# Kernel optimization log

Measured on AMD Instinct MI355X. Metric: run time of the kernel, lower is better.

## Reference

```python
import jax, jax.numpy as jnp
import numpy as np

# Fixed LeNet C3 connection table: input channel i feeds these 10 output channels.
CONN = [[0, 4, 5, 6, 9, 10, 11, 12, 14, 15],
        [0, 1, 5, 6, 7, 10, 11, 12, 13, 15],
        [0, 1, 2, 6, 7, 8, 11, 13, 14, 15],
        [1, 2, 3, 6, 7, 8, 9, 12, 14, 15],
        [2, 3, 4, 7, 8, 9, 10, 12, 13, 15],
        [3, 4, 5, 8, 9, 10, 11, 13, 14, 15]]
# Static scatter indices: (out_channel, in_channel) pairs, 60 total.
_ROWS = np.concatenate([np.asarray(l, np.int32) for l in CONN])  # out-channel ids
_COLS = np.repeat(np.arange(6, dtype=np.int32), 10)              # in-channel ids


def setup_inputs() -> dict:
    key = jax.random.key(0)
    k1, k2 = jax.random.split(key)
    x = jax.random.normal(k1, (64, 6, 256, 256), jnp.float32)
    # kaiming-uniform-ish scale for 6*5*5 fan-in
    weight = jax.random.normal(k2, (10, 6, 5, 5), jnp.float32) * 0.1
    bias = jnp.full((1, 16, 1, 1), 0.01, jnp.float32)
    return {"x": x, "weight": weight, "bias": bias}


def reference(x, weight, bias):
    # Fold the per-input-channel loop + scatter-add into one dense [16,6,5,5]
    # kernel with zeros where the connection table is absent. Each iteration i
    # of the original adds conv(x[:,i], weight[j,i]) to out channel CONN[i][j].
    w_flat = weight.transpose(1, 0, 2, 3).reshape(60, 5, 5)  # ordered (i, j)
    w_full = jnp.zeros((16, 6, 5, 5), weight.dtype).at[_ROWS, _COLS].set(w_flat)
    # Bias for channel c is added once per list containing c -> multiply by count.
    counts = jnp.zeros((16,), weight.dtype).at[_ROWS].add(1.0)
    out = jax.lax.conv_general_dilated(
        x, w_full, window_strides=(1, 1), padding='VALID',
        dimension_numbers=('NCHW', 'OIHW', 'NCHW'))
    return out + bias * counts.reshape(1, 16, 1, 1)
```

## Files before the change

kernel.cpp:

```cpp
#include <hip/hip_runtime.h>
#include <hip/hip_fp16.h>

typedef _Float16 f16x8 __attribute__((ext_vector_type(8)));
typedef float f32x4 __attribute__((ext_vector_type(4)));

__device__ constexpr int CONN[6][10] = {
    {0, 4, 5, 6, 9, 10, 11, 12, 14, 15},
    {0, 1, 5, 6, 7, 10, 11, 12, 13, 15},
    {0, 1, 2, 6, 7, 8, 11, 13, 14, 15},
    {1, 2, 3, 6, 7, 8, 9, 12, 14, 15},
    {2, 3, 4, 7, 8, 9, 10, 12, 13, 15},
    {3, 4, 5, 8, 9, 10, 11, 13, 14, 15}};

__device__ constexpr int CNT[16] = {3,3,3,3,3,3,4,4,4,4,4,4,4,4,4,6};

__device__ __forceinline__ f16x8 u4_to_h8(uint4 u) { f16x8 r; __builtin_memcpy(&r, &u, 16); return r; }

#define PITCH_DW 132
#define PLANE_DW (17 * 132)

__global__ void prep_A(const float* __restrict__ w, unsigned short* __restrict__ Wp) {
    int t = blockIdx.x * 256 + threadIdx.x;
    if (t >= 5120) return;
    int j = t & 7, lane = (t >> 3) & 63, ks = t >> 9;
    int ch = lane & 15, kb = lane >> 4;
    float val = 0.f;
    if (kb < 3 && j < 5) {
        int ii = 2 * kb + (ks >= 5 ? 1 : 0);
        int r  = (ks >= 5) ? ks - 5 : ks;
        for (int jj = 0; jj < 10; ++jj)
            if (CONN[ii][jj] == ch) val = w[jj * 150 + ii * 25 + r * 5 + j];
    }
    __half h = __float2half(val);
    unsigned short u; __builtin_memcpy(&u, &h, 2);
    Wp[t] = u;
}

__global__ __launch_bounds__(256, 3) void c3_mfma(
    const float* __restrict__ x, const unsigned short* __restrict__ Wp,
    const float* __restrict__ bias, float* __restrict__ out)
{
    __shared__ unsigned s_lds[6 * PLANE_DW];

    const int tid = threadIdx.x;
    const int id = (blockIdx.x & 7) * 168 + (blockIdx.x >> 3);
    const int by = id % 21;
    const int n  = id / 21;
    const int Y0 = by * 12;
    const float* xin = x + (size_t)n * 6 * 65536;

    #pragma unroll 4
    for (int it = 0; it < 24; ++it) {
        int i   = tid + it * 256;
        int c4  = i & 63;
        int row = (i >> 6) & 15;
        int ch  = i >> 10;
        float4 v = *reinterpret_cast<const float4*>(
            xin + (size_t)ch * 65536 + (size_t)(Y0 + row) * 256 + c4 * 4);
        __half2 lo = __floats2half2_rn(v.x, v.y);
        __half2 hi = __floats2half2_rn(v.z, v.w);
        uint2 u; __builtin_memcpy(&u.x, &lo, 4); __builtin_memcpy(&u.y, &hi, 4);
        *reinterpret_cast<uint2*>(&s_lds[ch * PLANE_DW + row * PITCH_DW + c4 * 2]) = u;
    }
    if (tid < 96) {
        int ch = tid >> 4, row = tid & 15;
        *reinterpret_cast<uint2*>(&s_lds[ch * PLANE_DW + row * PITCH_DW + 128]) =
            make_uint2(0u, 0u);
    }
    __syncthreads();

    const int lane = tid & 63;
    const int wv   = tid >> 6;
    const int nn   = lane & 15;
    const int kb   = lane >> 4;

    f16x8 W[10];
    const uint4* wp4 = reinterpret_cast<const uint4*>(Wp);
    #pragma unroll
    for (int ks = 0; ks < 10; ++ks) W[ks] = u4_to_h8(wp4[ks * 64 + lane]);

    const int iiA = (kb < 3) ? 2 * kb : 0;
    const unsigned shb = (unsigned)((nn & 1) * 16);

    auto loadf = [&](int dwaddr) -> f16x8 {
        unsigned e0 = s_lds[dwaddr],     e1 = s_lds[dwaddr + 1],
                 e2 = s_lds[dwaddr + 2], e3 = s_lds[dwaddr + 3],
                 e4 = s_lds[dwaddr + 4];
        unsigned o0 = (unsigned)((((unsigned long long)e1 << 32) | e0) >> shb);
        unsigned o1 = (unsigned)((((unsigned long long)e2 << 32) | e1) >> shb);
        unsigned o2 = (unsigned)((((unsigned long long)e3 << 32) | e2) >> shb);
        unsigned o3 = (unsigned)((((unsigned long long)e4 << 32) | e3) >> shb);
        return u4_to_h8(make_uint4(o0, o1, o2, o3));
    };

    float bb[4];
    #pragma unroll
    for (int q = 0; q < 4; ++q) {
        int ch = kb * 4 + q;
        bb[q] = bias[ch] * (float)CNT[ch];
    }

#define PHASE(a0,a1,a2,a3,a4,b0,b1,b2,b3,b4)                                    \
    {                                                                           \
        f32x4 accA = {bb[0], bb[1], bb[2], bb[3]};                              \
        f32x4 accB = {0.f, 0.f, 0.f, 0.f};                                      \
        accA = __builtin_amdgcn_mfma_f32_16x16x32_f16(W[0], a0, accA, 0, 0, 0); \
        accB = __builtin_amdgcn_mfma_f32_16x16x32_f16(W[5], b0, accB, 0, 0, 0); \
        a0 = loadf(aN); b0 = loadf(aN + 2244); aN += PITCH_DW;                  \
        accA = __builtin_amdgcn_mfma_f32_16x16x32_f16(W[1], a1, accA, 0, 0, 0); \
        accB = __builtin_amdgcn_mfma_f32_16x16x32_f16(W[6], b1, accB, 0, 0, 0); \
        accA = __builtin_amdgcn_mfma_f32_16x16x32_f16(W[2], a2, accA, 0, 0, 0); \
        accB = __builtin_amdgcn_mfma_f32_16x16x32_f16(W[7], b2, accB, 0, 0, 0); \
        accA = __builtin_amdgcn_mfma_f32_16x16x32_f16(W[3], a3, accA, 0, 0, 0); \
        accB = __builtin_amdgcn_mfma_f32_16x16x32_f16(W[8], b3, accB, 0, 0, 0); \
        accA = __builtin_amdgcn_mfma_f32_16x16x32_f16(W[4], a4, accA, 0, 0, 0); \
        accB = __builtin_amdgcn_mfma_f32_16x16x32_f16(W[9], b4, accB, 0, 0, 0); \
        if (xok) {                                                              \
            f32x4 acc = accA + accB;                                            \
            op0[0 * 63504 + yoff] = acc[0];                                     \
            op0[1 * 63504 + yoff] = acc[1];                                     \
            op0[2 * 63504 + yoff] = acc[2];                                     \
            op0[3 * 63504 + yoff] = acc[3];                                     \
        }                                                                       \
        yoff += 252;                                                            \
    }

    #pragma unroll 1
    for (int t = 0; t < 4; ++t) {
        const int gx = 64 * t + 16 * wv + nn;
        const bool xok = gx < 252;
        const int baseA = iiA * PLANE_DW + (gx >> 1);
        f16x8 A0 = loadf(baseA + 0 * PITCH_DW), A1 = loadf(baseA + 1 * PITCH_DW),
              A2 = loadf(baseA + 2 * PITCH_DW), A3 = loadf(baseA + 3 * PITCH_DW),
              A4 = loadf(baseA + 4 * PITCH_DW);
        f16x8 B0 = loadf(baseA + 2244 + 0 * PITCH_DW), B1 = loadf(baseA + 2244 + 1 * PITCH_DW),
              B2 = loadf(baseA + 2244 + 2 * PITCH_DW), B3 = loadf(baseA + 2244 + 3 * PITCH_DW),
              B4 = loadf(baseA + 2244 + 4 * PITCH_DW);
        int aN = baseA + 5 * PITCH_DW;

        float* const op0 = out + (size_t)n * 16 * 63504 + (size_t)(kb * 4) * 63504 + gx;
        int yoff = Y0 * 252;

        PHASE(A0, A1, A2, A3, A4, B0, B1, B2, B3, B4)
        PHASE(A1, A2, A3, A4, A0, B1, B2, B3, B4, B0)
        PHASE(A2, A3, A4, A0, A1, B2, B3, B4, B0, B1)
        PHASE(A3, A4, A0, A1, A2, B3, B4, B0, B1, B2)
        PHASE(A4, A0, A1, A2, A3, B4, B0, B1, B2, B3)
        PHASE(A0, A1, A2, A3, A4, B0, B1, B2, B3, B4)
        PHASE(A1, A2, A3, A4, A0, B1, B2, B3, B4, B0)
        PHASE(A2, A3, A4, A0, A1, B2, B3, B4, B0, B1)
        PHASE(A3, A4, A0, A1, A2, B3, B4, B0, B1, B2)
        PHASE(A4, A0, A1, A2, A3, B4, B0, B1, B2, B3)
        PHASE(A0, A1, A2, A3, A4, B0, B1, B2, B3, B4)
        PHASE(A1, A2, A3, A4, A0, B1, B2, B3, B4, B0)
    }
#undef PHASE
}

extern "C" void kernel_launch(void* const* d_in, const int* in_sizes, int n_in,
                              void* d_out, int out_size, void* d_ws, size_t ws_size,
                              hipStream_t stream) {
    const float* x    = (const float*)d_in[0];
    const float* w    = (const float*)d_in[1];
    const float* bias = (const float*)d_in[2];
    float* out = (float*)d_out;
    unsigned short* Wp = (unsigned short*)d_ws;

    hipLaunchKernelGGL(prep_A, dim3(20), dim3(256), 0, stream, w, Wp);
    hipLaunchKernelGGL(c3_mfma, dim3(1344), dim3(256), 0, stream, x, Wp, bias, out);
}
```

Baseline: 110.3 us.

## Switch conv inner loop to 32x32x16 MFMA with three-plane K slices

Replaces the paired 16x16x32 MFMA accumulators with a single 32x32x16 MFMA chain. Each wave now covers 32 output columns and three input planes per K half, and the weights are repacked into 15 K-slices. LDS reads switch to 64-bit aligned loads with odd/even selection, and plane padding is adjusted. This is meant to cut MFMA issue and LDS instruction counts per output. In exchange, half of the 32x32 accumulator rows are wasted (only 16 channels), and register pressure rises.

```diff
diff --git a/kernel.cpp b/kernel.cpp
--- a/kernel.cpp
+++ b/kernel.cpp
@@ -2,7 +2,7 @@
 #include <hip/hip_fp16.h>
 
 typedef _Float16 f16x8 __attribute__((ext_vector_type(8)));
-typedef float f32x4 __attribute__((ext_vector_type(4)));
+typedef float f32x16 __attribute__((ext_vector_type(16)));
 
 __device__ constexpr int CONN[6][10] = {
     {0, 4, 5, 6, 9, 10, 11, 12, 14, 15},
@@ -17,20 +17,20 @@
 __device__ __forceinline__ f16x8 u4_to_h8(uint4 u) { f16x8 r; __builtin_memcpy(&r, &u, 16); return r; }
 
 #define PITCH_DW 132
-#define PLANE_DW (17 * 132)
+#define PLANE_DW 2128
+#define LDS_DW   (6 * 2128 + 140)
 
 __global__ void prep_A(const float* __restrict__ w, unsigned short* __restrict__ Wp) {
     int t = blockIdx.x * 256 + threadIdx.x;
-    if (t >= 5120) return;
-    int j = t & 7, lane = (t >> 3) & 63, ks = t >> 9;
-    int ch = lane & 15, kb = lane >> 4;
+    if (t >= 7680) return;
+    int j = t & 7, lane = (t >> 3) & 63, ms = t >> 9;
+    int ch = lane & 31, kb = lane >> 5;
+    int slice = ms + 15 * kb;
+    int ii = slice / 5, r = slice % 5;
     float val = 0.f;
-    if (kb < 3 && j < 5) {
-        int ii = 2 * kb + (ks >= 5 ? 1 : 0);
-        int r  = (ks >= 5) ? ks - 5 : ks;
+    if (ch < 16 && j < 5)
         for (int jj = 0; jj < 10; ++jj)
             if (CONN[ii][jj] == ch) val = w[jj * 150 + ii * 25 + r * 5 + j];
-    }
     __half h = __float2half(val);
     unsigned short u; __builtin_memcpy(&u, &h, 2);
     Wp[t] = u;
@@ -40,7 +40,7 @@
     const float* __restrict__ x, const unsigned short* __restrict__ Wp,
     const float* __restrict__ bias, float* __restrict__ out)
 {
-    __shared__ unsigned s_lds[6 * PLANE_DW];
+    __shared__ unsigned s_lds[LDS_DW];
 
     const int tid = threadIdx.x;
     const int id = (blockIdx.x & 7) * 168 + (blockIdx.x >> 3);
@@ -64,97 +64,116 @@
     }
     if (tid < 96) {
         int ch = tid >> 4, row = tid & 15;
-        *reinterpret_cast<uint2*>(&s_lds[ch * PLANE_DW + row * PITCH_DW + 128]) =
-            make_uint2(0u, 0u);
+        *reinterpret_cast<uint4*>(&s_lds[ch * PLANE_DW + row * PITCH_DW + 128]) =
+            make_uint4(0u, 0u, 0u, 0u);
     }
     __syncthreads();
 
     const int lane = tid & 63;
     const int wv   = tid >> 6;
-    const int nn   = lane & 15;
-    const int kb   = lane >> 4;
+    const int nn   = lane & 31;
+    const int kb   = lane >> 5;
 
-    f16x8 W[10];
+    f16x8 W[15];
     const uint4* wp4 = reinterpret_cast<const uint4*>(Wp);
     #pragma unroll
-    for (int ks = 0; ks < 10; ++ks) W[ks] = u4_to_h8(wp4[ks * 64 + lane]);
+    for (int ms = 0; ms < 15; ++ms) W[ms] = u4_to_h8(wp4[ms * 64 + lane]);
 
-    const int iiA = (kb < 3) ? 2 * kb : 0;
+    f32x16 cinit;
+    #pragma unroll
+    for (int reg = 0; reg < 8; ++reg) {
+        int ch = (reg & 3) + 8 * (reg >> 2) + 4 * kb;
+        cinit[reg] = bias[ch] * (float)CNT[ch];
+    }
+    #pragma unroll
+    for (int reg = 8; reg < 16; ++reg) cinit[reg] = 0.f;
+
     const unsigned shb = (unsigned)((nn & 1) * 16);
 
-    auto loadf = [&](int dwaddr) -> f16x8 {
-        unsigned e0 = s_lds[dwaddr],     e1 = s_lds[dwaddr + 1],
-                 e2 = s_lds[dwaddr + 2], e3 = s_lds[dwaddr + 3],
-                 e4 = s_lds[dwaddr + 4];
-        unsigned o0 = (unsigned)((((unsigned long long)e1 << 32) | e0) >> shb);
-        unsigned o1 = (unsigned)((((unsigned long long)e2 << 32) | e1) >> shb);
-        unsigned o2 = (unsigned)((((unsigned long long)e3 << 32) | e2) >> shb);
-        unsigned o3 = (unsigned)((((unsigned long long)e4 << 32) | e3) >> shb);
-        return u4_to_h8(make_uint4(o0, o1, o2, o3));
-    };
+#define MFMA32(a, b, c) __builtin_amdgcn_mfma_f32_32x32x16_f16(a, b, c, 0, 0, 0)
 
-    float bb[4];
-    #pragma unroll
-    for (int q = 0; q < 4; ++q) {
-        int ch = kb * 4 + q;
-        bb[q] = bias[ch] * (float)CNT[ch];
+    #pragma unroll 1
+    for (int st = 0; st < 2; ++st) {
+        const int gx  = (st * 4 + wv) * 32 + nn;
+        const bool xok = gx < 252;
+        const int pb  = 3 * kb * PLANE_DW + (gx >> 1);
+
+        auto loadf = [&](int dw) -> f16x8 {
+            int d0 = dw & ~1;
+            uint2 r0 = *reinterpret_cast<const uint2*>(&s_lds[d0]);
+            uint2 r1 = *reinterpret_cast<const uint2*>(&s_lds[d0 + 2]);
+            uint2 r2 = *reinterpret_cast<const uint2*>(&s_lds[d0 + 4]);
+            const bool odd = dw & 1;
+            unsigned e0 = odd ? r0.y : r0.x;
+            unsigned e1 = odd ? r1.x : r0.y;
+            unsigned e2 = odd ? r1.y : r1.x;
+            unsigned e3 = odd ? r2.x : r1.y;
+            unsigned e4 = odd ? r2.y : r2.x;
+            unsigned o0 = (unsigned)((((unsigned long long)e1 << 32) | e0) >> shb);
+            unsigned o1 = (unsigned)((((unsigned long long)e2 << 32) | e1) >> shb);
+            unsigned o2 = (unsigned)((((unsigned long long)e3 << 32) | e2) >> shb);
+            unsigned o3 = (unsigned)((((unsigned long long)e4 << 32) | e3) >> shb);
+            return u4_to_h8(make_uint4(o0, o1, o2, o3));
+        };
+
+        f16x8 F00 = loadf(pb + 0 * PITCH_DW), F01 = loadf(pb + 1 * PITCH_DW),
+              F02 = loadf(pb + 2 * PITCH_DW), F03 = loadf(pb + 3 * PITCH_DW),
+              F04 = loadf(pb + 4 * PITCH_DW);
+        f16x8 F10 = loadf(pb + PLANE_DW + 0 * PITCH_DW), F11 = loadf(pb + PLANE_DW + 1 * PITCH_DW),
+              F12 = loadf(pb + PLANE_DW + 2 * PITCH_DW), F13 = loadf(pb + PLANE_DW + 3 * PITCH_DW),
+              F14 = loadf(pb + PLANE_DW + 4 * PITCH_DW);
+        f16x8 F20 = loadf(pb + 2 * PLANE_DW + 0 * PITCH_DW), F21 = loadf(pb + 2 * PLANE_DW + 1 * PITCH_DW),
+              F22 = loadf(pb + 2 * PLANE_DW + 2 * PITCH_DW), F23 = loadf(pb + 2 * PLANE_DW + 3 * PITCH_DW),
+              F24 = loadf(pb + 2 * PLANE_DW + 4 * PITCH_DW);
+        int rowN = 5 * PITCH_DW;
+
+        float* const opg = out + (size_t)n * 16 * 63504 + (size_t)(4 * kb) * 63504 + gx;
+        int yoff = Y0 * 252;
+
+#define PHASE(f00,f01,f02,f03,f04, f10,f11,f12,f13,f14, f20,f21,f22,f23,f24)   \
+    {                                                                          \
+        f32x16 acc = cinit;                                                    \
+        acc = MFMA32(W[0],  f00, acc);  acc = MFMA32(W[1],  f01, acc);         \
+        acc = MFMA32(W[2],  f02, acc);  acc = MFMA32(W[3],  f03, acc);         \
+        acc = MFMA32(W[4],  f04, acc);                                         \
+        acc = MFMA32(W[5],  f10, acc);  acc = MFMA32(W[6],  f11, acc);         \
+        acc = MFMA32(W[7],  f12, acc);  acc = MFMA32(W[8],  f13, acc);         \
+        acc = MFMA32(W[9],  f14, acc);                                         \
+        acc = MFMA32(W[10], f20, acc);  acc = MFMA32(W[11], f21, acc);         \
+        acc = MFMA32(W[12], f22, acc);  acc = MFMA32(W[13], f23, acc);         \
+        acc = MFMA32(W[14], f24, acc);                                         \
+        if (xok) {                                                             \
+            opg[yoff +  0 * 63504] = acc[0];                                   \
+            opg[yoff +  1 * 63504] = acc[1];                                   \
+            opg[yoff +  2 * 63504] = acc[2];                                   \
+            opg[yoff +  3 * 63504] = acc[3];                                   \
+            opg[yoff +  8 * 63504] = acc[4];                                   \
+            opg[yoff +  9 * 63504] = acc[5];                                   \
+            opg[yoff + 10 * 63504] = acc[6];                                   \
+            opg[yoff + 11 * 63504] = acc[7];                                   \
+        }                                                                      \
+        yoff += 252;                                                           \
+        f00 = loadf(pb + rowN);                                                \
+        f10 = loadf(pb + PLANE_DW + rowN);                                     \
+        f20 = loadf(pb + 2 * PLANE_DW + rowN);                                 \
+        rowN += PITCH_DW;                                                      \
     }
 
-#define PHASE(a0,a1,a2,a3,a4,b0,b1,b2,b3,b4)                                    \
-    {                                                                           \
-        f32x4 accA = {bb[0], bb[1], bb[2], bb[3]};                              \
-        f32x4 accB = {0.f, 0.f, 0.f, 0.f};                                      \
-        accA = __builtin_amdgcn_mfma_f32_16x16x32_f16(W[0], a0, accA, 0, 0, 0); \
-        accB = __builtin_amdgcn_mfma_f32_16x16x32_f16(W[5], b0, accB, 0, 0, 0); \
-        a0 = loadf(aN); b0 = loadf(aN + 2244); aN += PITCH_DW;                  \
-        accA = __builtin_amdgcn_mfma_f32_16x16x32_f16(W[1], a1, accA, 0, 0, 0); \
-        accB = __builtin_amdgcn_mfma_f32_16x16x32_f16(W[6], b1, accB, 0, 0, 0); \
-        accA = __builtin_amdgcn_mfma_f32_16x16x32_f16(W[2], a2, accA, 0, 0, 0); \
-        accB = __builtin_amdgcn_mfma_f32_16x16x32_f16(W[7], b2, accB, 0, 0, 0); \
-        accA = __builtin_amdgcn_mfma_f32_16x16x32_f16(W[3], a3, accA, 0, 0, 0); \
-        accB = __builtin_amdgcn_mfma_f32_16x16x32_f16(W[8], b3, accB, 0, 0, 0); \
-        accA = __builtin_amdgcn_mfma_f32_16x16x32_f16(W[4], a4, accA, 0, 0, 0); \
-        accB = __builtin_amdgcn_mfma_f32_16x16x32_f16(W[9], b4, accB, 0, 0, 0); \
-        if (xok) {                                                              \
-            f32x4 acc = accA + accB;                                            \
-            op0[0 * 63504 + yoff] = acc[0];                                     \
-            op0[1 * 63504 + yoff] = acc[1];                                     \
-            op0[2 * 63504 + yoff] = acc[2];                                     \
-            op0[3 * 63504 + yoff] = acc[3];                                     \
-        }                                                                       \
-        yoff += 252;                                                            \
+        PHASE(F00,F01,F02,F03,F04, F10,F11,F12,F13,F14, F20,F21,F22,F23,F24)
+        PHASE(F01,F02,F03,F04,F00, F11,F12,F13,F14,F10, F21,F22,F23,F24,F20)
+        PHASE(F02,F03,F04,F00,F01, F12,F13,F14,F10,F11, F22,F23,F24,F20,F21)
+        PHASE(F03,F04,F00,F01,F02, F13,F14,F10,F11,F12, F23,F24,F20,F21,F22)
+        PHASE(F04,F00,F01,F02,F03, F14,F10,F11,F12,F13, F24,F20,F21,F22,F23)
+        PHASE(F00,F01,F02,F03,F04, F10,F11,F12,F13,F14, F20,F21,F22,F23,F24)
+        PHASE(F01,F02,F03,F04,F00, F11,F12,F13,F14,F10, F21,F22,F23,F24,F20)
+        PHASE(F02,F03,F04,F00,F01, F12,F13,F14,F10,F11, F22,F23,F24,F20,F21)
+        PHASE(F03,F04,F00,F01,F02, F13,F14,F10,F11,F12, F23,F24,F20,F21,F22)
+        PHASE(F04,F00,F01,F02,F03, F14,F10,F11,F12,F13, F24,F20,F21,F22,F23)
+        PHASE(F00,F01,F02,F03,F04, F10,F11,F12,F13,F14, F20,F21,F22,F23,F24)
+        PHASE(F01,F02,F03,F04,F00, F11,F12,F13,F14,F10, F21,F22,F23,F24,F20)
+#undef PHASE
     }
-
-    #pragma unroll 1
-    for (int t = 0; t < 4; ++t) {
-        const int gx = 64 * t + 16 * wv + nn;
-        const bool xok = gx < 252;
-        const int baseA = iiA * PLANE_DW + (gx >> 1);
-        f16x8 A0 = loadf(baseA + 0 * PITCH_DW), A1 = loadf(baseA + 1 * PITCH_DW),
-              A2 = loadf(baseA + 2 * PITCH_DW), A3 = loadf(baseA + 3 * PITCH_DW),
-              A4 = loadf(baseA + 4 * PITCH_DW);
-        f16x8 B0 = loadf(baseA + 2244 + 0 * PITCH_DW), B1 = loadf(baseA + 2244 + 1 * PITCH_DW),
-              B2 = loadf(baseA + 2244 + 2 * PITCH_DW), B3 = loadf(baseA + 2244 + 3 * PITCH_DW),
-              B4 = loadf(baseA + 2244 + 4 * PITCH_DW);
-        int aN = baseA + 5 * PITCH_DW;
-
-        float* const op0 = out + (size_t)n * 16 * 63504 + (size_t)(kb * 4) * 63504 + gx;
-        int yoff = Y0 * 252;
-
-        PHASE(A0, A1, A2, A3, A4, B0, B1, B2, B3, B4)
-        PHASE(A1, A2, A3, A4, A0, B1, B2, B3, B4, B0)
-        PHASE(A2, A3, A4, A0, A1, B2, B3, B4, B0, B1)
-        PHASE(A3, A4, A0, A1, A2, B3, B4, B0, B1, B2)
-        PHASE(A4, A0, A1, A2, A3, B4, B0, B1, B2, B3)
-        PHASE(A0, A1, A2, A3, A4, B0, B1, B2, B3, B4)
-        PHASE(A1, A2, A3, A4, A0, B1, B2, B3, B4, B0)
-        PHASE(A2, A3, A4, A0, A1, B2, B3, B4, B0, B1)
-        PHASE(A3, A4, A0, A1, A2, B3, B4, B0, B1, B2)
-        PHASE(A4, A0, A1, A2, A3, B4, B0, B1, B2, B3)
-        PHASE(A0, A1, A2, A3, A4, B0, B1, B2, B3, B4)
-        PHASE(A1, A2, A3, A4, A0, B1, B2, B3, B4, B0)
-    }
-#undef PHASE
+#undef MFMA32
 }
 
 extern "C" void kernel_launch(void* const* d_in, const int* in_sizes, int n_in,
@@ -166,6 +185,6 @@
     float* out = (float*)d_out;
     unsigned short* Wp = (unsigned short*)d_ws;
 
-    hipLaunchKernelGGL(prep_A, dim3(20), dim3(256), 0, stream, w, Wp);
+    hipLaunchKernelGGL(prep_A, dim3(30), dim3(256), 0, stream, w, Wp);
     hipLaunchKernelGGL(c3_mfma, dim3(1344), dim3(256), 0, stream, x, Wp, bias, out);
 }
```

After: 116.5 us. 1.06x slower.

## Fuse weight prep into conv kernel and widen blocks to 16 waves

Applied to the files above, without the earlier changes.

Drops the separate weight-packing kernel. Each block now builds the fp16 MFMA weight panel in shared memory from the raw weights. Blocks grow from 256 to 1024 threads so each of the 16 waves handles one 16-column strip, replacing the per-wave loop over 4 column tiles. The LDS row pitch shrinks to 128 dwords with no zero padding, relying on masked columns and zero weight taps to absorb over-reads. This removes one launch and adds waves per CU, at the cost of redundant per-block weight packing and a heavier block barrier.

```diff
diff --git a/kernel.cpp b/kernel.cpp
--- a/kernel.cpp
+++ b/kernel.cpp
@@ -16,31 +16,17 @@
 
 __device__ __forceinline__ f16x8 u4_to_h8(uint4 u) { f16x8 r; __builtin_memcpy(&r, &u, 16); return r; }
 
-#define PITCH_DW 132
-#define PLANE_DW (17 * 132)
+#define PITCH_DW 128
+#define PLANE_DW 2048
+#define PANEL_DW 12288
+#define LDS_DW   14848
 
-__global__ void prep_A(const float* __restrict__ w, unsigned short* __restrict__ Wp) {
-    int t = blockIdx.x * 256 + threadIdx.x;
-    if (t >= 5120) return;
-    int j = t & 7, lane = (t >> 3) & 63, ks = t >> 9;
-    int ch = lane & 15, kb = lane >> 4;
-    float val = 0.f;
-    if (kb < 3 && j < 5) {
-        int ii = 2 * kb + (ks >= 5 ? 1 : 0);
-        int r  = (ks >= 5) ? ks - 5 : ks;
-        for (int jj = 0; jj < 10; ++jj)
-            if (CONN[ii][jj] == ch) val = w[jj * 150 + ii * 25 + r * 5 + j];
-    }
-    __half h = __float2half(val);
-    unsigned short u; __builtin_memcpy(&u, &h, 2);
-    Wp[t] = u;
-}
-
-__global__ __launch_bounds__(256, 3) void c3_mfma(
-    const float* __restrict__ x, const unsigned short* __restrict__ Wp,
+__global__ __launch_bounds__(1024, 4) void c3_mfma(
+    const float* __restrict__ x, const float* __restrict__ w,
     const float* __restrict__ bias, float* __restrict__ out)
 {
-    __shared__ unsigned s_lds[6 * PLANE_DW];
+    __shared__ unsigned s_lds[LDS_DW];
+    unsigned short* s_panel = reinterpret_cast<unsigned short*>(s_lds + PANEL_DW);
 
     const int tid = threadIdx.x;
     const int id = (blockIdx.x & 7) * 168 + (blockIdx.x >> 3);
@@ -49,9 +35,24 @@
     const int Y0 = by * 12;
     const float* xin = x + (size_t)n * 6 * 65536;
 
-    #pragma unroll 4
-    for (int it = 0; it < 24; ++it) {
-        int i   = tid + it * 256;
+    for (int t = tid; t < 5120; t += 1024) {
+        int j = t & 7, lane = (t >> 3) & 63, ks = t >> 9;
+        int ch = lane & 15, kb = lane >> 4;
+        float val = 0.f;
+        if (kb < 3 && j < 5) {
+            int ii = 2 * kb + (ks >= 5 ? 1 : 0);
+            int r  = (ks >= 5) ? ks - 5 : ks;
+            for (int jj = 0; jj < 10; ++jj)
+                if (CONN[ii][jj] == ch) val = w[jj * 150 + ii * 25 + r * 5 + j];
+        }
+        __half h = __float2half(val);
+        unsigned short u; __builtin_memcpy(&u, &h, 2);
+        s_panel[t] = u;
+    }
+
+    #pragma unroll
+    for (int it = 0; it < 6; ++it) {
+        int i   = tid + it * 1024;
         int c4  = i & 63;
         int row = (i >> 6) & 15;
         int ch  = i >> 10;
@@ -62,11 +63,6 @@
         uint2 u; __builtin_memcpy(&u.x, &lo, 4); __builtin_memcpy(&u.y, &hi, 4);
         *reinterpret_cast<uint2*>(&s_lds[ch * PLANE_DW + row * PITCH_DW + c4 * 2]) = u;
     }
-    if (tid < 96) {
-        int ch = tid >> 4, row = tid & 15;
-        *reinterpret_cast<uint2*>(&s_lds[ch * PLANE_DW + row * PITCH_DW + 128]) =
-            make_uint2(0u, 0u);
-    }
     __syncthreads();
 
     const int lane = tid & 63;
@@ -75,17 +71,22 @@
     const int kb   = lane >> 4;
 
     f16x8 W[10];
-    const uint4* wp4 = reinterpret_cast<const uint4*>(Wp);
-    #pragma unroll
-    for (int ks = 0; ks < 10; ++ks) W[ks] = u4_to_h8(wp4[ks * 64 + lane]);
+    {
+        const uint4* p4 = reinterpret_cast<const uint4*>(s_panel);
+        #pragma unroll
+        for (int ks = 0; ks < 10; ++ks) W[ks] = u4_to_h8(p4[ks * 64 + lane]);
+    }
 
     const int iiA = (kb < 3) ? 2 * kb : 0;
-    const unsigned shb = (unsigned)((nn & 1) * 16);
+    const int gx  = 16 * wv + nn;
+    const bool ok = gx < 252;
+    const int pb  = iiA * PLANE_DW + (gx >> 1);
+    const unsigned shb = (unsigned)((gx & 1) * 16);
 
-    auto loadf = [&](int dwaddr) -> f16x8 {
-        unsigned e0 = s_lds[dwaddr],     e1 = s_lds[dwaddr + 1],
-                 e2 = s_lds[dwaddr + 2], e3 = s_lds[dwaddr + 3],
-                 e4 = s_lds[dwaddr + 4];
+    auto loadf = [&](int dw) -> f16x8 {
+        unsigned e0 = s_lds[dw],     e1 = s_lds[dw + 1],
+                 e2 = s_lds[dw + 2], e3 = s_lds[dw + 3],
+                 e4 = s_lds[dw + 4];
         unsigned o0 = (unsigned)((((unsigned long long)e1 << 32) | e0) >> shb);
         unsigned o1 = (unsigned)((((unsigned long long)e2 << 32) | e1) >> shb);
         unsigned o2 = (unsigned)((((unsigned long long)e3 << 32) | e2) >> shb);
@@ -100,13 +101,24 @@
         bb[q] = bias[ch] * (float)CNT[ch];
     }
 
+    f16x8 A0 = loadf(pb + 0 * PITCH_DW), A1 = loadf(pb + 1 * PITCH_DW),
+          A2 = loadf(pb + 2 * PITCH_DW), A3 = loadf(pb + 3 * PITCH_DW),
+          A4 = loadf(pb + 4 * PITCH_DW);
+    f16x8 B0 = loadf(pb + PLANE_DW + 0 * PITCH_DW), B1 = loadf(pb + PLANE_DW + 1 * PITCH_DW),
+          B2 = loadf(pb + PLANE_DW + 2 * PITCH_DW), B3 = loadf(pb + PLANE_DW + 3 * PITCH_DW),
+          B4 = loadf(pb + PLANE_DW + 4 * PITCH_DW);
+    int aN = pb + 5 * PITCH_DW;
+
+    float* const op0 = out + (size_t)n * 16 * 63504 + (size_t)(kb * 4) * 63504 + gx;
+    int yoff = Y0 * 252;
+
 #define PHASE(a0,a1,a2,a3,a4,b0,b1,b2,b3,b4)                                    \
     {                                                                           \
         f32x4 accA = {bb[0], bb[1], bb[2], bb[3]};                              \
         f32x4 accB = {0.f, 0.f, 0.f, 0.f};                                      \
         accA = __builtin_amdgcn_mfma_f32_16x16x32_f16(W[0], a0, accA, 0, 0, 0); \
         accB = __builtin_amdgcn_mfma_f32_16x16x32_f16(W[5], b0, accB, 0, 0, 0); \
-        a0 = loadf(aN); b0 = loadf(aN + 2244); aN += PITCH_DW;                  \
+        a0 = loadf(aN); b0 = loadf(aN + PLANE_DW); aN += PITCH_DW;              \
         accA = __builtin_amdgcn_mfma_f32_16x16x32_f16(W[1], a1, accA, 0, 0, 0); \
         accB = __builtin_amdgcn_mfma_f32_16x16x32_f16(W[6], b1, accB, 0, 0, 0); \
         accA = __builtin_amdgcn_mfma_f32_16x16x32_f16(W[2], a2, accA, 0, 0, 0); \
@@ -115,7 +127,7 @@
         accB = __builtin_amdgcn_mfma_f32_16x16x32_f16(W[8], b3, accB, 0, 0, 0); \
         accA = __builtin_amdgcn_mfma_f32_16x16x32_f16(W[4], a4, accA, 0, 0, 0); \
         accB = __builtin_amdgcn_mfma_f32_16x16x32_f16(W[9], b4, accB, 0, 0, 0); \
-        if (xok) {                                                              \
+        if (ok) {                                                               \
             f32x4 acc = accA + accB;                                            \
             op0[0 * 63504 + yoff] = acc[0];                                     \
             op0[1 * 63504 + yoff] = acc[1];                                     \
@@ -125,35 +137,18 @@
         yoff += 252;                                                            \
     }
 
-    #pragma unroll 1
-    for (int t = 0; t < 4; ++t) {
-        const int gx = 64 * t + 16 * wv + nn;
-        const bool xok = gx < 252;
-        const int baseA = iiA * PLANE_DW + (gx >> 1);
-        f16x8 A0 = loadf(baseA + 0 * PITCH_DW), A1 = loadf(baseA + 1 * PITCH_DW),
-              A2 = loadf(baseA + 2 * PITCH_DW), A3 = loadf(baseA + 3 * PITCH_DW),
-              A4 = loadf(baseA + 4 * PITCH_DW);
-        f16x8 B0 = loadf(baseA + 2244 + 0 * PITCH_DW), B1 = loadf(baseA + 2244 + 1 * PITCH_DW),
-              B2 = loadf(baseA + 2244 + 2 * PITCH_DW), B3 = loadf(baseA + 2244 + 3 * PITCH_DW),
-              B4 = loadf(baseA + 2244 + 4 * PITCH_DW);
-        int aN = baseA + 5 * PITCH_DW;
-
-        float* const op0 = out + (size_t)n * 16 * 63504 + (size_t)(kb * 4) * 63504 + gx;
-        int yoff = Y0 * 252;
-
-        PHASE(A0, A1, A2, A3, A4, B0, B1, B2, B3, B4)
-        PHASE(A1, A2, A3, A4, A0, B1, B2, B3, B4, B0)
-        PHASE(A2, A3, A4, A0, A1, B2, B3, B4, B0, B1)
-        PHASE(A3, A4, A0, A1, A2, B3, B4, B0, B1, B2)
-        PHASE(A4, A0, A1, A2, A3, B4, B0, B1, B2, B3)
-        PHASE(A0, A1, A2, A3, A4, B0, B1, B2, B3, B4)
-        PHASE(A1, A2, A3, A4, A0, B1, B2, B3, B4, B0)
-        PHASE(A2, A3, A4, A0, A1, B2, B3, B4, B0, B1)
-        PHASE(A3, A4, A0, A1, A2, B3, B4, B0, B1, B2)
-        PHASE(A4, A0, A1, A2, A3, B4, B0, B1, B2, B3)
-        PHASE(A0, A1, A2, A3, A4, B0, B1, B2, B3, B4)
-        PHASE(A1, A2, A3, A4, A0, B1, B2, B3, B4, B0)
-    }
+    PHASE(A0, A1, A2, A3, A4, B0, B1, B2, B3, B4)
+    PHASE(A1, A2, A3, A4, A0, B1, B2, B3, B4, B0)
+    PHASE(A2, A3, A4, A0, A1, B2, B3, B4, B0, B1)
+    PHASE(A3, A4, A0, A1, A2, B3, B4, B0, B1, B2)
+    PHASE(A4, A0, A1, A2, A3, B4, B0, B1, B2, B3)
+    PHASE(A0, A1, A2, A3, A4, B0, B1, B2, B3, B4)
+    PHASE(A1, A2, A3, A4, A0, B1, B2, B3, B4, B0)
+    PHASE(A2, A3, A4, A0, A1, B2, B3, B4, B0, B1)
+    PHASE(A3, A4, A0, A1, A2, B3, B4, B0, B1, B2)
+    PHASE(A4, A0, A1, A2, A3, B4, B0, B1, B2, B3)
+    PHASE(A0, A1, A2, A3, A4, B0, B1, B2, B3, B4)
+    PHASE(A1, A2, A3, A4, A0, B1, B2, B3, B4, B0)
 #undef PHASE
 }
 
@@ -164,8 +159,6 @@
     const float* w    = (const float*)d_in[1];
     const float* bias = (const float*)d_in[2];
     float* out = (float*)d_out;
-    unsigned short* Wp = (unsigned short*)d_ws;
 
-    hipLaunchKernelGGL(prep_A, dim3(20), dim3(256), 0, stream, w, Wp);
-    hipLaunchKernelGGL(c3_mfma, dim3(1344), dim3(256), 0, stream, x, Wp, bias, out);
+    hipLaunchKernelGGL(c3_mfma, dim3(1344), dim3(1024), 0, stream, x, w, bias, out);
 }
```

Result: slower. 133.7 us (+21.2%).
